# Performance work log

Hardware: AMD Instinct MI355X
Metric: run time of the kernel (lower is better)

The kernel has to match this reference:

```python
import jax, jax.numpy as jnp
import numpy as np

N_MOL = 1024
ATOMS_PER_MOL = 100
ONLY_UNIQUE_PAIRS = False


def _build_pairs(asi_np: np.ndarray, only_unique: bool = ONLY_UNIQUE_PAIRS) -> np.ndarray:
    """Vectorized (host-side) segmented all-pairs enumeration, faithful to
    Pairlist.enumerate_all_pairs: for each molecule, every ordered pair (i, j)
    with i != j (or i < j if only_unique). The ragged index construction is
    static metadata (like the torch python loops), done once in numpy."""
    repeats = np.bincount(asi_np)                              # atoms per molecule
    offsets = np.concatenate(([0], np.cumsum(repeats)[:-1]))   # first atom of each molecule
    sizes_per_atom = repeats[asi_np]                           # r_m for each atom's molecule
    n = asi_np.shape[0]
    total = int(sizes_per_atom.sum())                          # sum of r_m^2 over molecules
    # i repeated r_m times per atom (matches repeat_interleave in torch code)
    i_idx = np.repeat(np.arange(n, dtype=np.int64), sizes_per_atom)
    # j sweeps arange(o_m, o_m + r_m) within each atom's block
    block_starts = np.concatenate(([0], np.cumsum(sizes_per_atom)[:-1]))
    j_idx = (np.arange(total, dtype=np.int64)
             - np.repeat(block_starts, sizes_per_atom)
             + np.repeat(offsets[asi_np], sizes_per_atom))
    mask = (i_idx < j_idx) if only_unique else (i_idx != j_idx)
    return np.stack((i_idx[mask], j_idx[mask]))                # (2, n_pairs)


def setup_inputs() -> dict:
    key = jax.random.key(0)
    n = N_MOL * ATOMS_PER_MOL
    positions = jax.random.normal(key, (n, 3), dtype=jnp.float32) * 10.0
    # sequential molecule ids 0..N_MOL-1, no gaps (required by the module)
    atomic_subsystem_indices = jnp.repeat(
        jnp.arange(N_MOL, dtype=jnp.int32), ATOMS_PER_MOL
    )
    return {"positions": positions,
            "atomic_subsystem_indices": atomic_subsystem_indices}


def reference(positions, atomic_subsystem_indices):
    asi_np = np.asarray(jax.device_get(atomic_subsystem_indices))
    pair_indices = jnp.asarray(_build_pairs(asi_np))           # (2, n_pairs) int64
    # r_ij = x_j - x_i (matches selected_positions[1] - selected_positions[0])
    r_ij = positions[pair_indices[1]] - positions[pair_indices[0]]  # (n_pairs, 3)
    d_ij = jnp.linalg.norm(r_ij, axis=1, keepdims=True)             # (n_pairs, 1)
    return pair_indices, d_ij, r_ij
```

## Files before the change

### kernel.cpp

```cpp
#include <hip/hip_runtime.h>


#define N_MOL 1024
#define APM   100
#define PPM   (APM * (APM-1))
#define NP    (N_MOL * PPM)

__global__ __launch_bounds__(256) void pairlist_kernel(
    const float* __restrict__ pos,
    float* __restrict__ out)
{
    int p = blockIdx.x * blockDim.x + threadIdx.x;
    if (p >= NP) return;

    unsigned up = (unsigned)p;
    unsigned m  = up / (unsigned)PPM;
    unsigned r  = up - m * (unsigned)PPM;
    unsigned il = r / 99u;
    unsigned k  = r - il * 99u;
    unsigned jl = k + (k >= il ? 1u : 0u);
    unsigned i  = m * (unsigned)APM + il;
    unsigned j  = m * (unsigned)APM + jl;

    float xi = pos[3u*i + 0u], yi = pos[3u*i + 1u], zi = pos[3u*i + 2u];
    float xj = pos[3u*j + 0u], yj = pos[3u*j + 1u], zj = pos[3u*j + 2u];

    float rx = xj - xi, ry = yj - yi, rz = zj - zi;
    float d  = sqrtf(rx*rx + ry*ry + rz*rz);

    out[p]          = (float)i;
    out[NP + p]     = (float)j;
    out[2*NP + p]   = d;

    float* rr = out + (size_t)3 * NP;
    size_t b = (size_t)3 * (size_t)p;
    rr[b + 0] = rx;
    rr[b + 1] = ry;
    rr[b + 2] = rz;
}

extern "C" void kernel_launch(void* const* d_in, const int* in_sizes, int n_in,
                              void* d_out, int out_size, void* d_ws, size_t ws_size,
                              hipStream_t stream) {
    const float* pos = (const float*)d_in[0];
    float* out = (float*)d_out;
    int nblocks = (NP + 255) / 256;
    pairlist_kernel<<<nblocks, 256, 0, stream>>>(pos, out);
}
```

Baseline: 41.47 us.

## Reassign threads to output float4 chunks for fully vectorized stores

Each thread now writes one aligned float4 of the output buffer. Threads are assigned by output region (i, j, d, or the interleaved r_ij), so each recomputes the pair indices and positions it needs. This replaces six scalar stores per pair, including strided stride-3 stores for r_ij, with coalesced 16-byte stores. In exchange there is redundant index decoding and position loading, plus divergence at region boundaries.

```diff
diff --git a/kernel.cpp b/kernel.cpp
--- a/kernel.cpp
+++ b/kernel.cpp
@@ -2,41 +2,71 @@
 
 
 #define N_MOL 1024
-#define APM   100
-#define PPM   (APM * (APM-1))
-#define NP    (N_MOL * PPM)
+#define APM   100u
+#define PPM   9900u
+#define NP    10137600u
+#define S4    (NP / 4u)
+#define NB    59400
+
+__device__ __forceinline__ void pair_decode(unsigned p, unsigned& i, unsigned& j) {
+    unsigned m  = p / PPM;
+    unsigned r  = p - m * PPM;
+    unsigned il = r / 99u;
+    unsigned k  = r - il * 99u;
+    unsigned jl = k + (k >= il ? 1u : 0u);
+    i = m * APM + il;
+    j = m * APM + jl;
+}
+
+__device__ __forceinline__ float3 pair_r(const float* __restrict__ pos, unsigned p) {
+    unsigned i, j;
+    pair_decode(p, i, j);
+    float xi = pos[3u*i+0u], yi = pos[3u*i+1u], zi = pos[3u*i+2u];
+    float xj = pos[3u*j+0u], yj = pos[3u*j+1u], zj = pos[3u*j+2u];
+    return make_float3(xj - xi, yj - yi, zj - zi);
+}
 
 __global__ __launch_bounds__(256) void pairlist_kernel(
     const float* __restrict__ pos,
     float* __restrict__ out)
 {
-    int p = blockIdx.x * blockDim.x + threadIdx.x;
-    if (p >= NP) return;
+    unsigned g = blockIdx.x * 256u + threadIdx.x;
+    float4 v;
 
-    unsigned up = (unsigned)p;
-    unsigned m  = up / (unsigned)PPM;
-    unsigned r  = up - m * (unsigned)PPM;
-    unsigned il = r / 99u;
-    unsigned k  = r - il * 99u;
-    unsigned jl = k + (k >= il ? 1u : 0u);
-    unsigned i  = m * (unsigned)APM + il;
-    unsigned j  = m * (unsigned)APM + jl;
+    if (g < S4) {
+        unsigned p0 = g * 4u;
+        #pragma unroll
+        for (int q = 0; q < 4; ++q) {
+            unsigned i, j; pair_decode(p0 + q, i, j);
+            ((float*)&v)[q] = (float)i;
+        }
+    } else if (g < 2u*S4) {
+        unsigned p0 = (g - S4) * 4u;
+        #pragma unroll
+        for (int q = 0; q < 4; ++q) {
+            unsigned i, j; pair_decode(p0 + q, i, j);
+            ((float*)&v)[q] = (float)j;
+        }
+    } else if (g < 3u*S4) {
+        unsigned p0 = (g - 2u*S4) * 4u;
+        #pragma unroll
+        for (int q = 0; q < 4; ++q) {
+            float3 r = pair_r(pos, p0 + q);
+            ((float*)&v)[q] = sqrtf(r.x*r.x + r.y*r.y + r.z*r.z);
+        }
+    } else {
+        unsigned u  = g - 3u*S4;
+        unsigned f0 = u * 4u;
+        unsigned p0 = f0 / 3u;
+        unsigned c0 = f0 - 3u*p0;
+        float3 a = pair_r(pos, p0);
+        float3 b = pair_r(pos, p0 + 1u);
+        if (c0 == 0u)      v = make_float4(a.x, a.y, a.z, b.x);
+        else if (c0 == 1u) v = make_float4(a.y, a.z, b.x, b.y);
+        else               v = make_float4(a.z, b.x, b.y, b.z);
+    }
 
-    float xi = pos[3u*i + 0u], yi = pos[3u*i + 1u], zi = pos[3u*i + 2u];
-    float xj = pos[3u*j + 0u], yj = pos[3u*j + 1u], zj = pos[3u*j + 2u];
-
-    float rx = xj - xi, ry = yj - yi, rz = zj - zi;
-    float d  = sqrtf(rx*rx + ry*ry + rz*rz);
-
-    out[p]          = (float)i;
-    out[NP + p]     = (float)j;
-    out[2*NP + p]   = d;
-
-    float* rr = out + (size_t)3 * NP;
-    size_t b = (size_t)3 * (size_t)p;
-    rr[b + 0] = rx;
-    rr[b + 1] = ry;
-    rr[b + 2] = rz;
+    ((float4*)out)[g] = v;
 }
 
 extern "C" void kernel_launch(void* const* d_in, const int* in_sizes, int n_in,
@@ -44,6 +74,5 @@
                               hipStream_t stream) {
     const float* pos = (const float*)d_in[0];
     float* out = (float*)d_out;
-    int nblocks = (NP + 255) / 256;
-    pairlist_kernel<<<nblocks, 256, 0, stream>>>(pos, out);
+    pairlist_kernel<<<NB, 256, 0, stream>>>(pos, out);
 }
```

Result: slower. 85.55 us (+106.3%).
